# Kernel optimization log

Hardware: AMD Instinct MI355X
Metric: run time of the kernel (lower is better)

Reference implementation:

```python
import jax, jax.numpy as jnp
import numpy as np

NQ = 12  # num_qubits
NL = 4   # num_layers (StronglyEntanglingLayers depth)
BATCH = 512


def _rx(a):
    # RX(a) = [[cos(a/2), -i sin(a/2)], [-i sin(a/2), cos(a/2)]]; a: (...,) float -> (...,2,2) complex64
    c = jnp.cos(a / 2)
    s = jnp.sin(a / 2)
    return jnp.stack([jnp.stack([c + 0j, -1j * s], -1),
                      jnp.stack([-1j * s, c + 0j], -1)], -2)


def _rot(phi, theta, omega):
    # Pennylane Rot(phi,theta,omega) = RZ(omega) RY(theta) RZ(phi)
    ct = jnp.cos(theta / 2)
    st = jnp.sin(theta / 2)
    ep = jnp.exp(-0.5j * (phi + omega))   # e^{-i(phi+omega)/2}
    em = jnp.exp(-0.5j * (phi - omega))   # e^{-i(phi-omega)/2}
    return jnp.stack([jnp.stack([ep * ct, -jnp.conj(em) * st], -1),
                      jnp.stack([em * st, jnp.conj(ep) * ct], -1)], -2)


def _apply_1q_shared(state, U, q):
    # state: (B,) + (2,)*n; U: (2,2) shared across batch
    s = jnp.moveaxis(state, q + 1, -1)
    s = s @ U.T
    return jnp.moveaxis(s, -1, q + 1)


def _apply_1q_batched(state, U, q):
    # U: (B,2,2), one gate per batch element (AngleEmbedding)
    s = jnp.moveaxis(state, q + 1, -1)
    s = jnp.einsum('b...i,bij->b...j', s, U)
    return jnp.moveaxis(s, -1, q + 1)


def _apply_cnot(state, c, t):
    # flip target axis on the control=1 slice
    s = jnp.moveaxis(state, (c + 1, t + 1), (1, 2))  # (B,2,2,rest)
    s = jnp.stack([s[:, 0], s[:, 1, ::-1]], axis=1)
    return jnp.moveaxis(s, (1, 2), (c + 1, t + 1))


def _circuit(batch_inputs, weights):
    B, n = batch_inputs.shape
    state = jnp.zeros((B, 2 ** n), jnp.complex64).at[:, 0].set(1.0)
    state = state.reshape((B,) + (2,) * n)
    # AngleEmbedding: RX(x_i) on wire i
    Ux = _rx(batch_inputs)  # (B,n,2,2)
    for q in range(n):
        state = _apply_1q_batched(state, Ux[:, q], q)
    # StronglyEntanglingLayers: per layer Rot on each wire then CNOT ring with range r
    Ur = _rot(weights[..., 0], weights[..., 1], weights[..., 2])  # (L,n,2,2)
    for l in range(NL):
        for q in range(n):
            state = _apply_1q_shared(state, Ur[l, q], q)
        r = (l % (n - 1)) + 1  # pennylane default ranges
        for q in range(n):
            state = _apply_cnot(state, q, (q + r) % n)
    # <Z_q> = p(0 on q) - p(1 on q)
    probs = state.real ** 2 + state.imag ** 2
    zs = []
    for q in range(n):
        p = jnp.moveaxis(probs, q + 1, 1).reshape(B, 2, -1).sum(-1)
        zs.append(p[:, 0] - p[:, 1])
    return jnp.stack(zs, axis=1)  # (B,n) float32


def setup_inputs() -> dict:
    key = jax.random.key(0)
    k1, k2, k3, k4 = jax.random.split(key, 4)
    return {
        'batch_inputs': jax.random.normal(k1, (BATCH, NQ), dtype=jnp.float32),
        'weights': jax.random.normal(k2, (NL, NQ, 3), dtype=jnp.float32),
        'head_w': jax.random.normal(k3, (1, NQ), dtype=jnp.float32) / np.sqrt(NQ),
        'head_b': jax.random.normal(k4, (1,), dtype=jnp.float32),
    }


def reference(batch_inputs, weights, head_w, head_b):
    expvals = _circuit(batch_inputs, weights)      # (B, NQ)
    return (expvals @ head_w.T + head_b)[:, 0]     # (B,)
```

## Files before the change

### kernel.cpp

```cpp
#include <hip/hip_runtime.h>

#define NQ 12
#define NL 4
#define NT 512

typedef float f32x2 __attribute__((ext_vector_type(2)));

constexpr unsigned gmap_f(int l, unsigned v) {
    int r = l + 1; unsigned x = v;
    for (int q = NQ - 1; q >= 0; --q) {
        int cb = NQ - 1 - q, tw = (q + r) % NQ, tb = NQ - 1 - tw;
        x ^= ((x >> cb) & 1u) << tb;
    }
    return x;
}
constexpr unsigned ginv_f(int l, unsigned v) {
    int r = l + 1; unsigned x = v;
    for (int q = 0; q < NQ; ++q) {
        int cb = NQ - 1 - q, tw = (q + r) % NQ, tb = NQ - 1 - tw;
        x ^= ((x >> cb) & 1u) << tb;
    }
    return x;
}
constexpr unsigned phi_f(unsigned x) { return x ^ ((x >> 4) & 14u) ^ ((x >> 8) & 14u); }

constexpr int POS[5][12] = {
    {0,1,2,3,4,5,6,7,8,9,10,11},
    {9,10,11,0,1,2,3,4,5,6,7,8},
    {0,1,2,9,5,6,10,7,8,11,3,4},
    {0,4,5,1,6,7,2,8,9,3,10,11},
    {0,9,2,4,1,10,3,5,11,6,7,8},
};
constexpr int DBITS[3][3] = { {0,1,2}, {3,6,9}, {8,10,11} };

constexpr unsigned pv(int t, unsigned v) { unsigned r = 0; for (int b = 0; b < 12; ++b) if ((v >> b) & 1) r |= 1u << POS[t][b]; return r; }
constexpr int bitat(int t, int i) { for (int b = 0; b < 12; ++b) if (POS[t][b] == i) return b; return -1; }
constexpr unsigned rowmask(int l, int b) { unsigned r = 0; for (int j = 0; j < 12; ++j) if ((gmap_f(l, 1u << j) >> b) & 1) r |= 1u << j; return r; }

struct Tabs {
    unsigned lcol[4][9];
    unsigned scol[4][8];
    int      gq[4][9];
    unsigned dm[3][3];
    unsigned dr[3][3];
    int      dg[3][3];
    unsigned rfin[12];
};
constexpr Tabs make_tabs() {
    Tabs T{};
    for (int t = 0; t <= 3; ++t) {
        for (int i = 3; i < 12; ++i)
            T.lcol[t][i - 3] = phi_f(pv(t + 1, ginv_f(t, 1u << bitat(t, i)))) << 3;
        for (int s = 0; s < 8; ++s) {
            unsigned v = 0;
            for (int bp = 0; bp < 3; ++bp)
                if ((s >> bp) & 1) v ^= phi_f(pv(t + 1, ginv_f(t, 1u << bitat(t, bp)))) << 3;
            T.scol[t][s] = v;
        }
        for (int i = 0; i < 9; ++i)
            T.gq[t][i] = t * NQ + (11 - bitat(t, i));
    }
    for (int t = 2; t <= 4; ++t)
        for (int j = 0; j < 3; ++j) {
            const int b = DBITS[t - 2][j];
            T.dm[t - 2][j] = pv(t, ginv_f(t - 1, 1u << b));
            T.dr[t - 2][j] = pv(t, rowmask(t - 1, b));
            T.dg[t - 2][j] = (t - 1) * NQ + (11 - b);
        }
    for (int q = 0; q < 12; ++q) T.rfin[q] = 1u << POS[4][11 - q];
    return T;
}
constexpr Tabs CT = make_tabs();

constexpr bool chk() {
    for (int t = 1; t <= 4; ++t) { unsigned seen = 0; for (int b = 0; b < 12; ++b) seen |= 1u << POS[t][b]; if (seen != 0xFFFu) return false; }
    for (int t = 1; t <= 3; ++t)
        for (int j = 0; j < 3; ++j) {
            if (POS[t][DBITS[t - 1][j]] < 9) return false;
            if (pv(t + 1, ginv_f(t, 1u << DBITS[t - 1][j])) >> 9) return false;
        }
    for (int j = 0; j < 3; ++j) if ((CT.dm[0][j] >> 3) > 31 || (CT.dm[1][j] >> 3) > 31 || (CT.dm[2][j] >> 3) > 31) return false;
    return true;
}
static_assert(chk(), "layout constraints violated");

template<int CTRL>
__device__ __forceinline__ f32x2 dpp2(f32x2 v) {
    f32x2 r;
    r.x = __int_as_float(__builtin_amdgcn_update_dpp(__float_as_int(v.x), __float_as_int(v.x), CTRL, 0xF, 0xF, false));
    r.y = __int_as_float(__builtin_amdgcn_update_dpp(__float_as_int(v.y), __float_as_int(v.y), CTRL, 0xF, 0xF, false));
    return r;
}
__device__ __forceinline__ void pswap32(f32x2 v, f32x2& lo, f32x2& hi) {
    float ax = v.x, bx = v.x;
    asm("v_permlane32_swap_b32 %0, %1" : "+v"(ax), "+v"(bx));
    float ay = v.y, by = v.y;
    asm("v_permlane32_swap_b32 %0, %1" : "+v"(ay), "+v"(by));
    lo = f32x2{ax, ay}; hi = f32x2{bx, by};
}
__device__ __forceinline__ void pswap16(f32x2 v, f32x2& ev, f32x2& od) {
    float ax = v.x, bx = v.x;
    asm("v_permlane16_swap_b32 %0, %1" : "+v"(ax), "+v"(bx));
    float ay = v.y, by = v.y;
    asm("v_permlane16_swap_b32 %0, %1" : "+v"(ay), "+v"(by));
    ev = f32x2{ax, ay}; od = f32x2{bx, by};
}
template<unsigned LAM>
__device__ __forceinline__ f32x2 lexch(f32x2 v, int lane) {
    f32x2 r = v;
    if constexpr (LAM & 16u) {
        f32x2 ev, od; pswap16(r, ev, od);
        r = (lane & 16) ? ev : od;
    }
    if constexpr (LAM & 8u) r = dpp2<0x128>(r);
    constexpr unsigned l7 = LAM & 7u;
    if constexpr (l7 == 1) r = dpp2<0xB1>(r);
    else if constexpr (l7 == 2) r = dpp2<0x4E>(r);
    else if constexpr (l7 == 3) r = dpp2<0x1B>(r);
    else if constexpr (l7 == 4) { r = dpp2<0x141>(r); r = dpp2<0x1B>(r); }
    else if constexpr (l7 == 5) { r = dpp2<0x141>(r); r = dpp2<0x4E>(r); }
    else if constexpr (l7 == 6) { r = dpp2<0x141>(r); r = dpp2<0xB1>(r); }
    else if constexpr (l7 == 7) r = dpp2<0x141>(r);
    return r;
}

template<int DI, int J>
__device__ __forceinline__ void deferred_gate(f32x2 rp[4], f32x2 ip[4], const float (*gm)[8],
                                              unsigned xbpos, int lane) {
    constexpr unsigned m = CT.dm[DI][J];
    constexpr unsigned r = CT.dr[DI][J];
    constexpr unsigned lam = m >> 3;
    constexpr unsigned s = m & 7u;
    constexpr int gi = CT.dg[DI][J];
    const float4 ga = *(const float4*)&gm[gi][0];
    const float4 gb = *(const float4*)&gm[gi][4];
    const int pt = __popc(xbpos & r) & 1;
    const float oA_r = pt ? gb.z : ga.x, oA_i = pt ? gb.w : ga.y;
    const float pA_r = pt ? gb.x : ga.z, pA_i = pt ? gb.y : ga.w;
    const float oB_r = pt ? ga.x : gb.z, oB_i = pt ? ga.y : gb.w;
    const float pB_r = pt ? ga.z : gb.x, pB_i = pt ? ga.w : gb.y;
    f32x2 nr[4], ni[4];
    #pragma unroll
    for (int k = 0; k < 4; ++k) {
        const int e0 = __builtin_popcount((unsigned)(2 * k) & (r & 7u)) & 1;
        const int e1 = e0 ^ (int)(r & 1u);
        const int ks = k ^ (int)(s >> 1);
        f32x2 per = lexch<lam>(rp[ks], lane);
        f32x2 pei = lexch<lam>(ip[ks], lane);
        if (s & 1u) { per = f32x2{per.y, per.x}; pei = f32x2{pei.y, pei.x}; }
        const f32x2 oR = f32x2{e0 ? oB_r : oA_r, e1 ? oB_r : oA_r};
        const f32x2 oI = f32x2{e0 ? oB_i : oA_i, e1 ? oB_i : oA_i};
        const f32x2 pR = f32x2{e0 ? pB_r : pA_r, e1 ? pB_r : pA_r};
        const f32x2 pI = f32x2{e0 ? pB_i : pA_i, e1 ? pB_i : pA_i};
        nr[k] = oR * rp[k] - oI * ip[k] + pR * per - pI * pei;
        ni[k] = oI * rp[k] + oR * ip[k] + pI * per + pR * pei;
    }
    #pragma unroll
    for (int k = 0; k < 4; ++k) { rp[k] = nr[k]; ip[k] = ni[k]; }
}

template<int P>
__device__ __forceinline__ void gates9(f32x2 rp[4], f32x2 ip[4], const float (*gm)[8], int lane) {
    {
        const float4 ga = *(const float4*)&gm[CT.gq[P][8]][0];
        const float4 gb = *(const float4*)&gm[CT.gq[P][8]][4];
        const int h = (lane >> 5) & 1;
        const float car = h ? gb.x : ga.x, cai = h ? gb.y : ga.y;
        const float cbr = h ? gb.z : ga.z, cbi = h ? gb.w : ga.w;
        #pragma unroll
        for (int k = 0; k < 4; ++k) {
            f32x2 r0r, r1r, r0i, r1i;
            pswap32(rp[k], r0r, r1r);
            pswap32(ip[k], r0i, r1i);
            rp[k] = car * r0r - cai * r0i + cbr * r1r - cbi * r1i;
            ip[k] = cai * r0r + car * r0i + cbi * r1r + cbr * r1i;
        }
    }
    {
        const float4 ga = *(const float4*)&gm[CT.gq[P][7]][0];
        const float4 gb = *(const float4*)&gm[CT.gq[P][7]][4];
        const int h = (lane >> 4) & 1;
        const float car = h ? gb.x : ga.x, cai = h ? gb.y : ga.y;
        const float cbr = h ? gb.z : ga.z, cbi = h ? gb.w : ga.w;
        #pragma unroll
        for (int k = 0; k < 4; ++k) {
            f32x2 r0r, r1r, r0i, r1i;
            pswap16(rp[k], r0r, r1r);
            pswap16(ip[k], r0i, r1i);
            rp[k] = car * r0r - cai * r0i + cbr * r1r - cbi * r1i;
            ip[k] = cai * r0r + car * r0i + cbi * r1r + cbr * r1i;
        }
    }
    {
        const float4 ga = *(const float4*)&gm[CT.gq[P][6]][0];
        const float4 gb = *(const float4*)&gm[CT.gq[P][6]][4];
        const int h = (lane >> 3) & 1;
        const float cMer = h ? gb.z : ga.x, cMei = h ? gb.w : ga.y;
        const float cOtr = h ? gb.x : ga.z, cOti = h ? gb.y : ga.w;
        #pragma unroll
        for (int k = 0; k < 4; ++k) {
            const f32x2 pR = dpp2<0x128>(rp[k]), pI = dpp2<0x128>(ip[k]);
            const f32x2 nr = cMer * rp[k] - cMei * ip[k] + cOtr * pR - cOti * pI;
            const f32x2 ni = cMei * rp[k] + cMer * ip[k] + cOti * pR + cOtr * pI;
            rp[k] = nr; ip[k] = ni;
        }
    }
    {
        const float4 ga = *(const float4*)&gm[CT.gq[P][5]][0];
        const float4 gb = *(const float4*)&gm[CT.gq[P][5]][4];
        const int h = (lane >> 2) & 1;
        const float cMer = h ? gb.z : ga.x, cMei = h ? gb.w : ga.y;
        const float cOtr = h ? gb.x : ga.z, cOti = h ? gb.y : ga.w;
        #pragma unroll
        for (int k = 0; k < 4; ++k) {
            const f32x2 pR = dpp2<0x1B>(dpp2<0x141>(rp[k]));
            const f32x2 pI = dpp2<0x1B>(dpp2<0x141>(ip[k]));
            const f32x2 nr = cMer * rp[k] - cMei * ip[k] + cOtr * pR - cOti * pI;
            const f32x2 ni = cMei * rp[k] + cMer * ip[k] + cOti * pR + cOtr * pI;
            rp[k] = nr; ip[k] = ni;
        }
    }
    {
        const float4 ga = *(const float4*)&gm[CT.gq[P][4]][0];
        const float4 gb = *(const float4*)&gm[CT.gq[P][4]][4];
        const int h = (lane >> 1) & 1;
        const float cMer = h ? gb.z : ga.x, cMei = h ? gb.w : ga.y;
        const float cOtr = h ? gb.x : ga.z, cOti = h ? gb.y : ga.w;
        #pragma unroll
        for (int k = 0; k < 4; ++k) {
            const f32x2 pR = dpp2<0x4E>(rp[k]), pI = dpp2<0x4E>(ip[k]);
            const f32x2 nr = cMer * rp[k] - cMei * ip[k] + cOtr * pR - cOti * pI;
            const f32x2 ni = cMei * rp[k] + cMer * ip[k] + cOti * pR + cOtr * pI;
            rp[k] = nr; ip[k] = ni;
        }
    }
    {
        const float4 ga = *(const float4*)&gm[CT.gq[P][3]][0];
        const float4 gb = *(const float4*)&gm[CT.gq[P][3]][4];
        const int h = lane & 1;
        const float cMer = h ? gb.z : ga.x, cMei = h ? gb.w : ga.y;
        const float cOtr = h ? gb.x : ga.z, cOti = h ? gb.y : ga.w;
        #pragma unroll
        for (int k = 0; k < 4; ++k) {
            const f32x2 pR = dpp2<0xB1>(rp[k]), pI = dpp2<0xB1>(ip[k]);
            const f32x2 nr = cMer * rp[k] - cMei * ip[k] + cOtr * pR - cOti * pI;
            const f32x2 ni = cMei * rp[k] + cMer * ip[k] + cOti * pR + cOtr * pI;
            rp[k] = nr; ip[k] = ni;
        }
    }
    {
        const float4 ga = *(const float4*)&gm[CT.gq[P][2]][0];
        const float4 gb = *(const float4*)&gm[CT.gq[P][2]][4];
        #pragma unroll
        for (int h2 = 0; h2 < 2; ++h2) {
            const int k0 = h2, k1 = h2 + 2;
            const f32x2 a0r = rp[k0], a0i = ip[k0], a1r = rp[k1], a1i = ip[k1];
            rp[k0] = ga.x * a0r - ga.y * a0i + ga.z * a1r - ga.w * a1i;
            ip[k0] = ga.y * a0r + ga.x * a0i + ga.w * a1r + ga.z * a1i;
            rp[k1] = gb.x * a0r - gb.y * a0i + gb.z * a1r - gb.w * a1i;
            ip[k1] = gb.y * a0r + gb.x * a0i + gb.w * a1r + gb.z * a1i;
        }
    }
    {
        const float4 ga = *(const float4*)&gm[CT.gq[P][1]][0];
        const float4 gb = *(const float4*)&gm[CT.gq[P][1]][4];
        #pragma unroll
        for (int h2 = 0; h2 < 2; ++h2) {
            const int k0 = 2 * h2, k1 = k0 + 1;
            const f32x2 a0r = rp[k0], a0i = ip[k0], a1r = rp[k1], a1i = ip[k1];
            rp[k0] = ga.x * a0r - ga.y * a0i + ga.z * a1r - ga.w * a1i;
            ip[k0] = ga.y * a0r + ga.x * a0i + ga.w * a1r + ga.z * a1i;
            rp[k1] = gb.x * a0r - gb.y * a0i + gb.z * a1r - gb.w * a1i;
            ip[k1] = gb.y * a0r + gb.x * a0i + gb.w * a1r + gb.z * a1i;
        }
    }
    {
        const float4 ga = *(const float4*)&gm[CT.gq[P][0]][0];
        const float4 gb = *(const float4*)&gm[CT.gq[P][0]][4];
        const f32x2 K0r = f32x2{ga.x, gb.x}, K0i = f32x2{ga.y, gb.y};
        const f32x2 K1r = f32x2{ga.z, gb.z}, K1i = f32x2{ga.w, gb.w};
        #pragma unroll
        for (int k = 0; k < 4; ++k) {
            const float a0r = rp[k].x, a0i = ip[k].x, a1r = rp[k].y, a1i = ip[k].y;
            rp[k] = K0r * a0r - K0i * a0i + K1r * a1r - K1i * a1i;
            ip[k] = K0i * a0r + K0r * a0i + K1i * a1r + K1r * a1i;
        }
    }
}

template<int P>
__device__ __forceinline__ void scatter_p(const f32x2 rp[4], const f32x2 ip[4], float2* wb, int lane, int wv) {
    unsigned sbase = 0;
    #pragma unroll
    for (int j = 0; j < 6; ++j) if ((lane >> j) & 1) sbase ^= CT.lcol[P][j];
    #pragma unroll
    for (int j = 0; j < 3; ++j) if ((wv >> j) & 1) sbase ^= CT.lcol[P][6 + j];
    #pragma unroll
    for (int k = 0; k < 4; ++k) {
        *(float2*)((char*)wb + (sbase ^ CT.scol[P][2 * k]))     = make_float2(rp[k].x, ip[k].x);
        *(float2*)((char*)wb + (sbase ^ CT.scol[P][2 * k + 1])) = make_float2(rp[k].y, ip[k].y);
    }
}

__device__ __forceinline__ void readst(f32x2 rp[4], f32x2 ip[4], const float2* rb, unsigned wbyte) {
    #pragma unroll
    for (int k = 0; k < 4; ++k) {
        const float4 v = *(const float4*)((const char*)rb + (wbyte ^ ((unsigned)k << 4)));
        rp[k] = f32x2{v.x, v.z}; ip[k] = f32x2{v.y, v.w};
    }
}

__global__ __launch_bounds__(NT, 8) void qsim_kernel(
    const float* __restrict__ xin,
    const float* __restrict__ wts,
    const float* __restrict__ hw,
    const float* __restrict__ hb,
    float* __restrict__ out)
{
    __shared__ alignas(16) float2 buf[4096];
    __shared__ float gm[NL * NQ][8];
    __shared__ float wred[8];

    const int tid  = threadIdx.x;
    const int lane = tid & 63;
    const int wv   = tid >> 6;
    const int b    = blockIdx.x;
    const int b11 = wv >> 2, b10 = (wv >> 1) & 1, b9 = wv & 1;

    if (tid < NL * NQ) {
        const float phi = wts[tid * 3 + 0];
        const float th  = wts[tid * 3 + 1];
        const float om  = wts[tid * 3 + 2];
        const float ct = cosf(0.5f * th), stt = sinf(0.5f * th);
        const float apo = -0.5f * (phi + om), amo = -0.5f * (phi - om);
        const float epr = cosf(apo), epi = sinf(apo);
        const float emr = cosf(amo), emi = sinf(amo);
        float* g = gm[tid];
        g[0] =  epr * ct;  g[1] =  epi * ct;
        g[2] = -emr * stt; g[3] =  emi * stt;
        g[4] =  emr * stt; g[5] =  emi * stt;
        g[6] =  epr * ct;  g[7] = -epi * ct;
    }

    float cv[NQ], sv[NQ];
    #pragma unroll
    for (int bp = 0; bp < NQ; ++bp) {
        const float a = 0.5f * xin[b * NQ + (NQ - 1 - bp)];
        cv[bp] = __cosf(a); sv[bp] = __sinf(a);
    }
    float MS[8];
    MS[0] = cv[0]; MS[1] = sv[0];
    #pragma unroll
    for (int bit = 1; bit < 3; ++bit) {
        #pragma unroll
        for (int j = (1 << bit) - 1; j >= 0; --j) {
            MS[j | (1 << bit)] = MS[j] * sv[bit];
            MS[j]              = MS[j] * cv[bit];
        }
    }

    const unsigned xbpos = ((unsigned)wv << 9) | ((unsigned)lane << 3);
    const unsigned wbyte = phi_f(xbpos) << 3;

    __syncthreads();

    f32x2 rp[4], ip[4];

    {
        const float* G0 = gm[0];
        const float* G1 = gm[1];
        const float* G2 = gm[2];
        const float w0r = G0[4 * b11] * cv[11]     + G0[4 * b11 + 3] * sv[11];
        const float w0i = G0[4 * b11 + 1] * cv[11] - G0[4 * b11 + 2] * sv[11];
        const float w1r = G1[4 * b10] * cv[10]     + G1[4 * b10 + 3] * sv[10];
        const float w1i = G1[4 * b10 + 1] * cv[10] - G1[4 * b10 + 2] * sv[10];
        const float w2r = G2[4 * b9] * cv[9]       + G2[4 * b9 + 3] * sv[9];
        const float w2i = G2[4 * b9 + 1] * cv[9]   - G2[4 * b9 + 2] * sv[9];
        const float t01r = w0r * w1r - w0i * w1i, t01i = w0r * w1i + w0i * w1r;
        float Ar = t01r * w2r - t01i * w2i;
        float Ai = t01r * w2i + t01i * w2r;
        float mm = 1.f;
        #pragma unroll
        for (int j = 0; j < 6; ++j) mm *= ((lane >> j) & 1) ? sv[3 + j] : cv[3 + j];
        Ar *= mm; Ai *= mm;
        const int pcl = __popc((unsigned)lane) & 3;
        float Br, Bi;
        if      (pcl == 0) { Br =  Ar; Bi =  Ai; }
        else if (pcl == 1) { Br =  Ai; Bi = -Ar; }
        else if (pcl == 2) { Br = -Ar; Bi = -Ai; }
        else               { Br = -Ai; Bi =  Ar; }
        #pragma unroll
        for (int s = 0; s < 8; ++s) {
            const float m = MS[s];
            const int pc = __builtin_popcount((unsigned)s) & 3;
            float ar, ai;
            if      (pc == 0) { ar =  Br * m; ai =  Bi * m; }
            else if (pc == 1) { ar =  Bi * m; ai = -Br * m; }
            else if (pc == 2) { ar = -Br * m; ai = -Bi * m; }
            else              { ar = -Bi * m; ai =  Br * m; }
            if (s & 1) { rp[s >> 1].y = ar; ip[s >> 1].y = ai; }
            else       { rp[s >> 1].x = ar; ip[s >> 1].x = ai; }
        }
        gates9<0>(rp, ip, gm, lane);
        scatter_p<0>(rp, ip, buf, lane, wv);
    }
    __syncthreads();

    readst(rp, ip, buf, wbyte);
    gates9<1>(rp, ip, gm, lane);
    __syncthreads();
    scatter_p<1>(rp, ip, buf, lane, wv);
    __syncthreads();

    readst(rp, ip, buf, wbyte);
    deferred_gate<0, 0>(rp, ip, gm, xbpos, lane);
    deferred_gate<0, 1>(rp, ip, gm, xbpos, lane);
    deferred_gate<0, 2>(rp, ip, gm, xbpos, lane);
    gates9<2>(rp, ip, gm, lane);
    __syncthreads();
    scatter_p<2>(rp, ip, buf, lane, wv);
    __syncthreads();

    readst(rp, ip, buf, wbyte);
    deferred_gate<1, 0>(rp, ip, gm, xbpos, lane);
    deferred_gate<1, 1>(rp, ip, gm, xbpos, lane);
    deferred_gate<1, 2>(rp, ip, gm, xbpos, lane);
    gates9<3>(rp, ip, gm, lane);
    __syncthreads();
    scatter_p<3>(rp, ip, buf, lane, wv);
    __syncthreads();

    {
        readst(rp, ip, buf, wbyte);
        deferred_gate<2, 0>(rp, ip, gm, xbpos, lane);
        deferred_gate<2, 1>(rp, ip, gm, xbpos, lane);
        deferred_gate<2, 2>(rp, ip, gm, xbpos, lane);

        float CS[8];
        #pragma unroll
        for (int s = 0; s < 8; ++s) CS[s] = 0.f;
        #pragma unroll
        for (int q = 0; q < NQ; ++q) {
            const unsigned m = CT.rfin[q];
            const float wq = (__popc(xbpos & m) & 1) ? -hw[q] : hw[q];
            #pragma unroll
            for (int s = 0; s < 8; ++s)
                CS[s] += (__builtin_popcount((unsigned)s & m) & 1) ? -wq : wq;
        }
        f32x2 acc = f32x2{0.f, 0.f};
        #pragma unroll
        for (int k = 0; k < 4; ++k) {
            const f32x2 pr = rp[k] * rp[k] + ip[k] * ip[k];
            acc += pr * f32x2{CS[2 * k], CS[2 * k + 1]};
        }
        float sres = acc.x + acc.y;
        #pragma unroll
        for (int off = 32; off >= 1; off >>= 1)
            sres += __shfl_xor(sres, off, 64);
        if (lane == 0) wred[wv] = sres;
        __syncthreads();
        if (tid == 0) {
            float s = hb[0];
            #pragma unroll
            for (int w = 0; w < 8; ++w) s += wred[w];
            out[b] = s;
        }
    }
}

extern "C" void kernel_launch(void* const* d_in, const int* in_sizes, int n_in,
                              void* d_out, int out_size, void* d_ws, size_t ws_size,
                              hipStream_t stream) {
    const float* x  = (const float*)d_in[0];
    const float* wt = (const float*)d_in[1];
    const float* hw = (const float*)d_in[2];
    const float* hb = (const float*)d_in[3];
    float* outp = (float*)d_out;
    const int B = in_sizes[0] / NQ;
    qsim_kernel<<<B, NT, 0, stream>>>(x, wt, hw, hb, outp);
}
```

Before: 31.47 us.

## Double-buffer LDS state to drop one barrier per stage; group head weights by mask

Uses two shared state buffers so each stage scatters into the buffer other than the one it just read. That removes the barrier that used to sit between the read and the scatter. It also sums head weights into eight buckets by their low three mask bits before building the per-slot signs, replacing a 12x8 inner loop. The cost is twice the shared memory per block, and launch bounds are relaxed from 8 to 4 blocks per CU, which may lower occupancy.

New measurement: 32.12 us. 2.1% more time.

```diff
diff --git a/kernel.cpp b/kernel.cpp
--- a/kernel.cpp
+++ b/kernel.cpp
@@ -310,14 +310,14 @@
     }
 }
 
-__global__ __launch_bounds__(NT, 8) void qsim_kernel(
+__global__ __launch_bounds__(NT, 4) void qsim_kernel(
     const float* __restrict__ xin,
     const float* __restrict__ wts,
     const float* __restrict__ hw,
     const float* __restrict__ hb,
     float* __restrict__ out)
 {
-    __shared__ alignas(16) float2 buf[4096];
+    __shared__ alignas(16) float2 buf[2][4096];
     __shared__ float gm[NL * NQ][8];
     __shared__ float wred[8];
 
@@ -402,51 +402,60 @@
             else       { rp[s >> 1].x = ar; ip[s >> 1].x = ai; }
         }
         gates9<0>(rp, ip, gm, lane);
-        scatter_p<0>(rp, ip, buf, lane, wv);
+        scatter_p<0>(rp, ip, buf[0], lane, wv);
     }
     __syncthreads();
 
-    readst(rp, ip, buf, wbyte);
+    readst(rp, ip, buf[0], wbyte);
     gates9<1>(rp, ip, gm, lane);
+    scatter_p<1>(rp, ip, buf[1], lane, wv);
     __syncthreads();
-    scatter_p<1>(rp, ip, buf, lane, wv);
-    __syncthreads();
-
-    readst(rp, ip, buf, wbyte);
+
+    readst(rp, ip, buf[1], wbyte);
     deferred_gate<0, 0>(rp, ip, gm, xbpos, lane);
     deferred_gate<0, 1>(rp, ip, gm, xbpos, lane);
     deferred_gate<0, 2>(rp, ip, gm, xbpos, lane);
     gates9<2>(rp, ip, gm, lane);
+    scatter_p<2>(rp, ip, buf[0], lane, wv);
     __syncthreads();
-    scatter_p<2>(rp, ip, buf, lane, wv);
-    __syncthreads();
-
-    readst(rp, ip, buf, wbyte);
+
+    readst(rp, ip, buf[0], wbyte);
     deferred_gate<1, 0>(rp, ip, gm, xbpos, lane);
     deferred_gate<1, 1>(rp, ip, gm, xbpos, lane);
     deferred_gate<1, 2>(rp, ip, gm, xbpos, lane);
     gates9<3>(rp, ip, gm, lane);
+    scatter_p<3>(rp, ip, buf[1], lane, wv);
     __syncthreads();
-    scatter_p<3>(rp, ip, buf, lane, wv);
-    __syncthreads();
-
-    {
-        readst(rp, ip, buf, wbyte);
+
+    {
+        readst(rp, ip, buf[1], wbyte);
         deferred_gate<2, 0>(rp, ip, gm, xbpos, lane);
         deferred_gate<2, 1>(rp, ip, gm, xbpos, lane);
         deferred_gate<2, 2>(rp, ip, gm, xbpos, lane);
 
+        float W[8] = {0.f,0.f,0.f,0.f,0.f,0.f,0.f,0.f};
+        #pragma unroll
+        for (int q = 0; q < NQ; ++q) {
+            constexpr unsigned m = 0;
+            (void)m;
+            const unsigned mq = CT.rfin[q];
+            const float wq = (__popc(xbpos & mq) & 1) ? -hw[q] : hw[q];
+            W[mq & 7u] += wq;
+        }
         float CS[8];
         #pragma unroll
-        for (int s = 0; s < 8; ++s) CS[s] = 0.f;
-        #pragma unroll
-        for (int q = 0; q < NQ; ++q) {
-            const unsigned m = CT.rfin[q];
-            const float wq = (__popc(xbpos & m) & 1) ? -hw[q] : hw[q];
-            #pragma unroll
-            for (int s = 0; s < 8; ++s)
-                CS[s] += (__builtin_popcount((unsigned)s & m) & 1) ? -wq : wq;
-        }
+        for (int s = 0; s < 8; ++s) {
+            float acc = W[0];
+            acc += ((s & 1) ? -W[1] : W[1]);
+            acc += ((s & 2) ? -W[2] : W[2]);
+            acc += ((__builtin_popcount((unsigned)(s & 3)) & 1) ? -W[3] : W[3]);
+            acc += ((s & 4) ? -W[4] : W[4]);
+            acc += ((__builtin_popcount((unsigned)(s & 5)) & 1) ? -W[5] : W[5]);
+            acc += ((__builtin_popcount((unsigned)(s & 6)) & 1) ? -W[6] : W[6]);
+            acc += ((__builtin_popcount((unsigned)(s & 7)) & 1) ? -W[7] : W[7]);
+            CS[s] = acc;
+        }
+
         f32x2 acc = f32x2{0.f, 0.f};
         #pragma unroll
         for (int k = 0; k < 4; ++k) {
```
